# Kernel tuning notes

Hardware: AMD Instinct MI355X
Metric: run time of the kernel (lower is better)

The kernel has to match this reference:

```python
import jax, jax.numpy as jnp
import numpy as np

N, M, D = 8192, 8192, 64

def setup_inputs() -> dict:
    key = jax.random.key(0)
    kx, ky = jax.random.split(key)
    x = jax.random.normal(kx, (N, D), dtype=jnp.float32)
    y = jax.random.normal(ky, (M, D), dtype=jnp.float32)
    return {"x": x, "y": y}

def reference(x, y):
    T = 1.0
    # Dmat = 2 - euclidean cdist(x, y), computed via the Gram trick.
    sq = (jnp.sum(x * x, axis=1)[:, None]
          + jnp.sum(y * y, axis=1)[None, :]
          - 2.0 * (x @ y.T))
    Dmat = 2.0 - jnp.sqrt(jnp.maximum(sq, 0.0))          # [N, M]
    logprob_rows = jax.nn.log_softmax(Dmat * T, axis=1)   # [N, M]
    logprob_cols = jax.nn.log_softmax(Dmat.T * T, axis=1) # [M, N]
    choice_rows = jnp.argmax(logprob_rows, axis=1)        # [N]
    choice_cols = jnp.argmax(logprob_cols, axis=1)        # [M]
    seq = jnp.arange(M, dtype=choice_cols.dtype)
    mutual = choice_rows[choice_cols] == seq              # [M] bool
    lp_rows = jnp.take_along_axis(logprob_rows, choice_rows[:, None], axis=1)[:, 0]  # [N]
    lp_cols = jnp.take_along_axis(logprob_cols, choice_cols[:, None], axis=1)[:, 0]  # [M]
    # Padded (jit-friendly) form of the boolean compaction: entries where
    # mutual is False are zeroed; mutual mask identifies valid matches.
    log_probs = jnp.where(mutual, lp_rows[choice_cols] + lp_cols, 0.0)  # [M]
    dmatches = jnp.stack([choice_cols, seq], axis=1)      # [M, 2]
    return (log_probs, dmatches, mutual)
```

## Files before the change

### kernel.cpp

```cpp
#include <hip/hip_runtime.h>
#include <stdint.h>

#define NROWS 8192
#define MCOLS 8192
#define DDIM  64

typedef _Float16 half8   __attribute__((ext_vector_type(8)));
typedef float    float8  __attribute__((ext_vector_type(8)));
typedef float    floatx4 __attribute__((ext_vector_type(4)));

__device__ __forceinline__ unsigned f2key(float f) {
  unsigned u = __float_as_uint(f);
  return (u & 0x80000000u) ? ~u : (u | 0x80000000u);
}
__device__ __forceinline__ float key2f(unsigned k) {
  unsigned u = (k & 0x80000000u) ? (k & 0x7fffffffu) : ~k;
  return __uint_as_float(u);
}

__global__ __launch_bounds__(256, 4) void mfma_tile_kernel(
    const float* __restrict__ x, const float* __restrict__ y,
    unsigned long long* __restrict__ row_key, float* __restrict__ row_sum,
    unsigned long long* __restrict__ col_key, float* __restrict__ col_sum)
{
  __shared__ unsigned long long lkey[256];
  __shared__ float              lsum[256];

  const int wave = threadIdx.x >> 6;
  const int lane = threadIdx.x & 63;
  const int l15  = lane & 15;
  const int grp  = lane >> 4;
  const int ap0  = blockIdx.y * 8 + wave * 2;
  const int ro   = ap0 * 16 + grp * 4;
  const int colbase = blockIdx.x * 256;

  lkey[threadIdx.x] = 0ull;
  lsum[threadIdx.x] = 0.0f;
  __syncthreads();

  half8 Ah[2][2], Al[2][2];
  float normA[2];
  #pragma unroll
  for (int p = 0; p < 2; ++p) {
    const float* ax = x + (size_t)((ap0 + p) * 16 + l15) * DDIM + grp * 8;
    float8 f0 = *(const float8*)ax;
    float8 f1 = *(const float8*)(ax + 32);
    float pa = 0.0f;
    #pragma unroll
    for (int j = 0; j < 8; ++j) {
      _Float16 h0 = (_Float16)f0[j];
      _Float16 h1 = (_Float16)f1[j];
      Ah[p][0][j] = h0;  Al[p][0][j] = (_Float16)((f0[j] - (float)h0) * 2048.0f);
      Ah[p][1][j] = h1;  Al[p][1][j] = (_Float16)((f1[j] - (float)h1) * 2048.0f);
      pa = fmaf(f0[j], f0[j], pa);
      pa = fmaf(f1[j], f1[j], pa);
    }
    pa += __shfl_xor(pa, 16);
    pa += __shfl_xor(pa, 32);
    normA[p] = pa;
  }

  float xne[8], rsum[8], rmax[8]; int ridx[8];
  #pragma unroll
  for (int s = 0; s < 8; ++s) {
    xne[s]  = __shfl(normA[s >> 2], grp * 4 + (s & 3));
    rsum[s] = 0.0f; rmax[s] = -3.4e38f; ridx[s] = 0;
  }

  for (int jt = 0; jt < 16; ++jt) {
    const int cpg = blockIdx.x * 16 + jt;
    const float* by = y + (size_t)(cpg * 16 + l15) * DDIM + grp * 8;
    float8 g0 = *(const float8*)by;
    float8 g1 = *(const float8*)(by + 32);

    half8 bh0, bh1, bl0, bl1;
    float pb = 0.0f;
    #pragma unroll
    for (int j = 0; j < 8; ++j) {
      _Float16 h0 = (_Float16)g0[j];
      _Float16 h1 = (_Float16)g1[j];
      bh0[j] = h0;  bl0[j] = (_Float16)((g0[j] - (float)h0) * 2048.0f);
      bh1[j] = h1;  bl1[j] = (_Float16)((g1[j] - (float)h1) * 2048.0f);
      pb = fmaf(g0[j], g0[j], pb);
      pb = fmaf(g1[j], g1[j], pb);
    }
    pb += __shfl_xor(pb, 16);
    pb += __shfl_xor(pb, 32);
    const float ync = pb;
    const int col = colbase + jt * 16 + l15;

    float csum = 0.0f, cmax = -3.4e38f; int cs8 = 0;
    #pragma unroll
    for (int p = 0; p < 2; ++p) {
      floatx4 c1 = {}, c2 = {};
      c1 = __builtin_amdgcn_mfma_f32_16x16x32_f16(Ah[p][0], bh0, c1, 0, 0, 0);
      c1 = __builtin_amdgcn_mfma_f32_16x16x32_f16(Ah[p][1], bh1, c1, 0, 0, 0);
      c2 = __builtin_amdgcn_mfma_f32_16x16x32_f16(Al[p][0], bh0, c2, 0, 0, 0);
      c2 = __builtin_amdgcn_mfma_f32_16x16x32_f16(Al[p][1], bh1, c2, 0, 0, 0);
      c2 = __builtin_amdgcn_mfma_f32_16x16x32_f16(Ah[p][0], bl0, c2, 0, 0, 0);
      c2 = __builtin_amdgcn_mfma_f32_16x16x32_f16(Ah[p][1], bl1, c2, 0, 0, 0);
      #pragma unroll
      for (int r = 0; r < 4; ++r) {
        const int s = p * 4 + r;
        float dot = fmaf(c2[r], (1.0f / 2048.0f), c1[r]);
        float sq  = fmaxf(fmaf(-2.0f, dot, xne[s] + ync), 0.0f);
        float d   = 2.0f - __builtin_amdgcn_sqrtf(sq);
        float e   = __expf(d);
        rsum[s] += e;  csum += e;
        if (d > rmax[s]) ridx[s] = col;
        rmax[s] = fmaxf(rmax[s], d);
        if (d > cmax) cs8 = s;
        cmax = fmaxf(cmax, d);
      }
    }

    int crow = ro + ((cs8 >> 2) << 4) + (cs8 & 3);
    unsigned long long ckey =
        ((unsigned long long)f2key(cmax) << 32) |
        (unsigned long long)(unsigned)(~(unsigned)crow);
    atomicMax(&lkey[jt * 16 + l15], ckey);
    atomicAdd(&lsum[jt * 16 + l15], csum);
  }

  unsigned long long rkk[8];
  #pragma unroll
  for (int s = 0; s < 8; ++s)
    rkk[s] = ((unsigned long long)f2key(rmax[s]) << 32) |
             (unsigned long long)(unsigned)(~(unsigned)ridx[s]);
  #pragma unroll
  for (int off = 1; off < 16; off <<= 1) {
    #pragma unroll
    for (int s = 0; s < 8; ++s) {
      rsum[s] += __shfl_xor(rsum[s], off);
      unsigned long long o = __shfl_xor(rkk[s], off);
      if (o > rkk[s]) rkk[s] = o;
    }
  }
  if (l15 == 0) {
    #pragma unroll
    for (int s = 0; s < 8; ++s) {
      int row = ro + ((s >> 2) << 4) + (s & 3);
      atomicMax(row_key + row, rkk[s]);
      atomicAdd(row_sum + row, rsum[s]);
    }
  }

  __syncthreads();
  {
    int col = colbase + threadIdx.x;
    atomicMax(col_key + col, lkey[threadIdx.x]);
    atomicAdd(col_sum + col, lsum[threadIdx.x]);
  }
}

__global__ void finalize_kernel(const unsigned long long* __restrict__ row_key,
                                const float* __restrict__ row_sum,
                                const unsigned long long* __restrict__ col_key,
                                const float* __restrict__ col_sum,
                                float* __restrict__ out)
{
  int j = blockIdx.x * 256 + threadIdx.x;
  if (j >= MCOLS) return;
  unsigned long long ck = col_key[j];
  int   ci   = (int)(~(unsigned)ck);
  float cmax = key2f((unsigned)(ck >> 32));
  float lp_col = cmax - logf(col_sum[j]);

  unsigned long long rk = row_key[ci];
  int   rj   = (int)(~(unsigned)rk);
  float rmax = key2f((unsigned)(rk >> 32));
  float lp_row = rmax - logf(row_sum[ci]);

  int mut = (rj == j);
  out[j]                 = mut ? (lp_row + lp_col) : 0.0f;
  out[MCOLS + 2 * j + 0] = (float)ci;
  out[MCOLS + 2 * j + 1] = (float)j;
  out[3 * MCOLS + j]     = mut ? 1.0f : 0.0f;
}

extern "C" void kernel_launch(void* const* d_in, const int* in_sizes, int n_in,
                              void* d_out, int out_size, void* d_ws, size_t ws_size,
                              hipStream_t stream) {
  const float* x = (const float*)d_in[0];
  const float* y = (const float*)d_in[1];
  float* out = (float*)d_out;

  char* ws = (char*)d_ws;
  unsigned long long* row_key = (unsigned long long*)(ws);
  unsigned long long* col_key = (unsigned long long*)(ws + 65536);
  float* row_sum = (float*)(ws + 131072);
  float* col_sum = (float*)(ws + 163840);

  hipMemsetAsync(ws, 0, 196608, stream);

  dim3 grid(MCOLS / 256, NROWS / 128);
  mfma_tile_kernel<<<grid, 256, 0, stream>>>(x, y, row_key, row_sum,
                                             col_key, col_sum);
  finalize_kernel<<<32, 256, 0, stream>>>(row_key, row_sum, col_key, col_sum, out);
}
```

Measured before the change: 141.5 us.

## Precompute fp16 hi/lo split of y in MFMA layout, halve rows per wave

Adds a pre-pass kernel that splits y once into fp16 high and low parts stored in MFMA operand order, computes the y row norms, and zeroes the accumulators in place of the memset. The main kernel then loads ready half8 operands instead of reconverting y in every row block, and each wave handles one 16-row tile instead of two. The grid doubles and launch bounds target higher occupancy. The trade is an extra launch, more workspace traffic, and less reuse of each y tile across rows, which means more col atomics.

```diff
diff --git a/kernel.cpp b/kernel.cpp
--- a/kernel.cpp
+++ b/kernel.cpp
@@ -6,6 +6,7 @@
 #define DDIM  64
 
 typedef _Float16 half8   __attribute__((ext_vector_type(8)));
+typedef _Float16 half4   __attribute__((ext_vector_type(4)));
 typedef float    float8  __attribute__((ext_vector_type(8)));
 typedef float    floatx4 __attribute__((ext_vector_type(4)));
 
@@ -18,8 +19,48 @@
   return __uint_as_float(u);
 }
 
-__global__ __launch_bounds__(256, 4) void mfma_tile_kernel(
-    const float* __restrict__ x, const float* __restrict__ y,
+__global__ void convert_y_kernel(const float* __restrict__ y,
+                                 _Float16* __restrict__ yh, _Float16* __restrict__ yl,
+                                 float* __restrict__ yn,
+                                 unsigned long long* __restrict__ rk,
+                                 unsigned long long* __restrict__ ck,
+                                 float* __restrict__ rs, float* __restrict__ cs) {
+  const int gid = blockIdx.x * 256 + threadIdx.x;
+  if (gid < NROWS) { rk[gid] = 0ull; rs[gid] = 0.0f; ck[gid] = 0ull; cs[gid] = 0.0f; }
+
+  const int row = gid >> 4;
+  const int tq  = gid & 15;
+  const int k0  = tq * 4;
+  float4 v = *(const float4*)(y + (size_t)row * DDIM + k0);
+
+  half4 hb, lb;
+  float s = 0.0f;
+  {
+    float f0 = v.x, f1 = v.y, f2 = v.z, f3 = v.w;
+    _Float16 h0 = (_Float16)f0, h1 = (_Float16)f1, h2 = (_Float16)f2, h3 = (_Float16)f3;
+    hb[0] = h0; hb[1] = h1; hb[2] = h2; hb[3] = h3;
+    lb[0] = (_Float16)((f0 - (float)h0) * 2048.0f);
+    lb[1] = (_Float16)((f1 - (float)h1) * 2048.0f);
+    lb[2] = (_Float16)((f2 - (float)h2) * 2048.0f);
+    lb[3] = (_Float16)((f3 - (float)h3) * 2048.0f);
+    s = fmaf(f0, f0, fmaf(f1, f1, fmaf(f2, f2, f3 * f3)));
+  }
+  const int pos = ((row >> 4) << 10) + ((k0 >> 5) << 9)
+                + ((((k0 >> 3) & 3) << 4) + (row & 15)) * 8 + (k0 & 7);
+  *(half4*)(yh + pos) = hb;
+  *(half4*)(yl + pos) = lb;
+
+  s += __shfl_down(s, 8);
+  s += __shfl_down(s, 4);
+  s += __shfl_down(s, 2);
+  s += __shfl_down(s, 1);
+  if (tq == 0) yn[row] = s;
+}
+
+__global__ __launch_bounds__(256, 8) void mfma_tile_kernel(
+    const float* __restrict__ x,
+    const _Float16* __restrict__ yh, const _Float16* __restrict__ yl,
+    const float* __restrict__ yn,
     unsigned long long* __restrict__ row_key, float* __restrict__ row_sum,
     unsigned long long* __restrict__ col_key, float* __restrict__ col_sum)
 {
@@ -30,19 +71,18 @@
   const int lane = threadIdx.x & 63;
   const int l15  = lane & 15;
   const int grp  = lane >> 4;
-  const int ap0  = blockIdx.y * 8 + wave * 2;
-  const int ro   = ap0 * 16 + grp * 4;
+  const int ap   = blockIdx.y * 4 + wave;
+  const int ro   = ap * 16 + grp * 4;
   const int colbase = blockIdx.x * 256;
 
   lkey[threadIdx.x] = 0ull;
   lsum[threadIdx.x] = 0.0f;
   __syncthreads();
 
-  half8 Ah[2][2], Al[2][2];
-  float normA[2];
-  #pragma unroll
-  for (int p = 0; p < 2; ++p) {
-    const float* ax = x + (size_t)((ap0 + p) * 16 + l15) * DDIM + grp * 8;
+  half8 Ah0, Ah1, Al0, Al1;
+  float normA;
+  {
+    const float* ax = x + (size_t)(ap * 16 + l15) * DDIM + grp * 8;
     float8 f0 = *(const float8*)ax;
     float8 f1 = *(const float8*)(ax + 32);
     float pa = 0.0f;
@@ -50,98 +90,81 @@
     for (int j = 0; j < 8; ++j) {
       _Float16 h0 = (_Float16)f0[j];
       _Float16 h1 = (_Float16)f1[j];
-      Ah[p][0][j] = h0;  Al[p][0][j] = (_Float16)((f0[j] - (float)h0) * 2048.0f);
-      Ah[p][1][j] = h1;  Al[p][1][j] = (_Float16)((f1[j] - (float)h1) * 2048.0f);
+      Ah0[j] = h0;  Al0[j] = (_Float16)((f0[j] - (float)h0) * 2048.0f);
+      Ah1[j] = h1;  Al1[j] = (_Float16)((f1[j] - (float)h1) * 2048.0f);
       pa = fmaf(f0[j], f0[j], pa);
       pa = fmaf(f1[j], f1[j], pa);
     }
     pa += __shfl_xor(pa, 16);
     pa += __shfl_xor(pa, 32);
-    normA[p] = pa;
-  }
-
-  float xne[8], rsum[8], rmax[8]; int ridx[8];
+    normA = pa;
+  }
+
+  float xne[4], rsum[4], rmax[4]; int ridx[4];
   #pragma unroll
-  for (int s = 0; s < 8; ++s) {
-    xne[s]  = __shfl(normA[s >> 2], grp * 4 + (s & 3));
-    rsum[s] = 0.0f; rmax[s] = -3.4e38f; ridx[s] = 0;
-  }
+  for (int r = 0; r < 4; ++r) {
+    xne[r]  = __shfl(normA, grp * 4 + r);
+    rsum[r] = 0.0f; rmax[r] = -3.4e38f; ridx[r] = 0;
+  }
+
+  const half8* yh8 = (const half8*)yh;
+  const half8* yl8 = (const half8*)yl;
 
   for (int jt = 0; jt < 16; ++jt) {
-    const int cpg = blockIdx.x * 16 + jt;
-    const float* by = y + (size_t)(cpg * 16 + l15) * DDIM + grp * 8;
-    float8 g0 = *(const float8*)by;
-    float8 g1 = *(const float8*)(by + 32);
-
-    half8 bh0, bh1, bl0, bl1;
-    float pb = 0.0f;
-    #pragma unroll
-    for (int j = 0; j < 8; ++j) {
-      _Float16 h0 = (_Float16)g0[j];
-      _Float16 h1 = (_Float16)g1[j];
-      bh0[j] = h0;  bl0[j] = (_Float16)((g0[j] - (float)h0) * 2048.0f);
-      bh1[j] = h1;  bl1[j] = (_Float16)((g1[j] - (float)h1) * 2048.0f);
-      pb = fmaf(g0[j], g0[j], pb);
-      pb = fmaf(g1[j], g1[j], pb);
-    }
-    pb += __shfl_xor(pb, 16);
-    pb += __shfl_xor(pb, 32);
-    const float ync = pb;
+    const size_t b0 = (size_t)(blockIdx.x * 16 + jt) * 128 + lane;
+    const half8 bh0 = yh8[b0], bh1 = yh8[b0 + 64];
+    const half8 bl0 = yl8[b0], bl1 = yl8[b0 + 64];
     const int col = colbase + jt * 16 + l15;
-
-    float csum = 0.0f, cmax = -3.4e38f; int cs8 = 0;
-    #pragma unroll
-    for (int p = 0; p < 2; ++p) {
-      floatx4 c1 = {}, c2 = {};
-      c1 = __builtin_amdgcn_mfma_f32_16x16x32_f16(Ah[p][0], bh0, c1, 0, 0, 0);
-      c1 = __builtin_amdgcn_mfma_f32_16x16x32_f16(Ah[p][1], bh1, c1, 0, 0, 0);
-      c2 = __builtin_amdgcn_mfma_f32_16x16x32_f16(Al[p][0], bh0, c2, 0, 0, 0);
-      c2 = __builtin_amdgcn_mfma_f32_16x16x32_f16(Al[p][1], bh1, c2, 0, 0, 0);
-      c2 = __builtin_amdgcn_mfma_f32_16x16x32_f16(Ah[p][0], bl0, c2, 0, 0, 0);
-      c2 = __builtin_amdgcn_mfma_f32_16x16x32_f16(Ah[p][1], bl1, c2, 0, 0, 0);
-      #pragma unroll
-      for (int r = 0; r < 4; ++r) {
-        const int s = p * 4 + r;
-        float dot = fmaf(c2[r], (1.0f / 2048.0f), c1[r]);
-        float sq  = fmaxf(fmaf(-2.0f, dot, xne[s] + ync), 0.0f);
-        float d   = 2.0f - __builtin_amdgcn_sqrtf(sq);
-        float e   = __expf(d);
-        rsum[s] += e;  csum += e;
-        if (d > rmax[s]) ridx[s] = col;
-        rmax[s] = fmaxf(rmax[s], d);
-        if (d > cmax) cs8 = s;
-        cmax = fmaxf(cmax, d);
-      }
-    }
-
-    int crow = ro + ((cs8 >> 2) << 4) + (cs8 & 3);
+    const float ync = yn[col];
+
+    floatx4 c1 = {}, c2 = {};
+    c1 = __builtin_amdgcn_mfma_f32_16x16x32_f16(Ah0, bh0, c1, 0, 0, 0);
+    c1 = __builtin_amdgcn_mfma_f32_16x16x32_f16(Ah1, bh1, c1, 0, 0, 0);
+    c2 = __builtin_amdgcn_mfma_f32_16x16x32_f16(Al0, bh0, c2, 0, 0, 0);
+    c2 = __builtin_amdgcn_mfma_f32_16x16x32_f16(Al1, bh1, c2, 0, 0, 0);
+    c2 = __builtin_amdgcn_mfma_f32_16x16x32_f16(Ah0, bl0, c2, 0, 0, 0);
+    c2 = __builtin_amdgcn_mfma_f32_16x16x32_f16(Ah1, bl1, c2, 0, 0, 0);
+
+    float csum = 0.0f, cmax = -3.4e38f; int cr = 0;
+    #pragma unroll
+    for (int r = 0; r < 4; ++r) {
+      float dot = fmaf(c2[r], (1.0f / 2048.0f), c1[r]);
+      float sq  = fmaxf(fmaf(-2.0f, dot, xne[r] + ync), 0.0f);
+      float d   = 2.0f - __builtin_amdgcn_sqrtf(sq);
+      float e   = __expf(d);
+      rsum[r] += e;  csum += e;
+      if (d > rmax[r]) ridx[r] = col;
+      rmax[r] = fmaxf(rmax[r], d);
+      if (d > cmax) cr = r;
+      cmax = fmaxf(cmax, d);
+    }
+
     unsigned long long ckey =
         ((unsigned long long)f2key(cmax) << 32) |
-        (unsigned long long)(unsigned)(~(unsigned)crow);
+        (unsigned long long)(unsigned)(~(unsigned)(ro + cr));
     atomicMax(&lkey[jt * 16 + l15], ckey);
     atomicAdd(&lsum[jt * 16 + l15], csum);
   }
 
-  unsigned long long rkk[8];
+  unsigned long long rkk[4];
   #pragma unroll
-  for (int s = 0; s < 8; ++s)
-    rkk[s] = ((unsigned long long)f2key(rmax[s]) << 32) |
-             (unsigned long long)(unsigned)(~(unsigned)ridx[s]);
+  for (int r = 0; r < 4; ++r)
+    rkk[r] = ((unsigned long long)f2key(rmax[r]) << 32) |
+             (unsigned long long)(unsigned)(~(unsigned)ridx[r]);
   #pragma unroll
   for (int off = 1; off < 16; off <<= 1) {
     #pragma unroll
-    for (int s = 0; s < 8; ++s) {
-      rsum[s] += __shfl_xor(rsum[s], off);
-      unsigned long long o = __shfl_xor(rkk[s], off);
-      if (o > rkk[s]) rkk[s] = o;
+    for (int r = 0; r < 4; ++r) {
+      rsum[r] += __shfl_xor(rsum[r], off);
+      unsigned long long o = __shfl_xor(rkk[r], off);
+      if (o > rkk[r]) rkk[r] = o;
     }
   }
   if (l15 == 0) {
     #pragma unroll
-    for (int s = 0; s < 8; ++s) {
-      int row = ro + ((s >> 2) << 4) + (s & 3);
-      atomicMax(row_key + row, rkk[s]);
-      atomicAdd(row_sum + row, rsum[s]);
+    for (int r = 0; r < 4; ++r) {
+      atomicMax(row_key + ro + r, rkk[r]);
+      atomicAdd(row_sum + ro + r, rsum[r]);
     }
   }
 
@@ -190,11 +213,14 @@
   unsigned long long* col_key = (unsigned long long*)(ws + 65536);
   float* row_sum = (float*)(ws + 131072);
   float* col_sum = (float*)(ws + 163840);
-
-  hipMemsetAsync(ws, 0, 196608, stream);
-
-  dim3 grid(MCOLS / 256, NROWS / 128);
-  mfma_tile_kernel<<<grid, 256, 0, stream>>>(x, y, row_key, row_sum,
-                                             col_key, col_sum);
+  float* yn      = (float*)(ws + 196608);
+  _Float16* yh = (_Float16*)(ws + 229376);
+  _Float16* yl = (_Float16*)(ws + 229376 + 1048576);
+
+  convert_y_kernel<<<512, 256, 0, stream>>>(y, yh, yl, yn,
+                                            row_key, col_key, row_sum, col_sum);
+  dim3 grid(MCOLS / 256, NROWS / 64);
+  mfma_tile_kernel<<<grid, 256, 0, stream>>>(x, yh, yl, yn,
+                                             row_key, row_sum, col_key, col_sum);
   finalize_kernel<<<32, 256, 0, stream>>>(row_key, row_sum, col_key, col_sum, out);
 }
```

Measured after the change: 175.3 us. 23.9% more time.
